# Performance work log

Measured on AMD Instinct MI355X. Metric: run time of the kernel, lower is better.

The kernel has to match this reference:

```python
import jax, jax.numpy as jnp
import numpy as np

B, T, H, D = 2, 2048, 8, 128
HID = H * D          # 1024
K_CONV = 4
EPS = 1e-5


def causal_dwconv(x, w, b):
    # x: [B,T,C], w: [C,K], b: [C]
    # torch Conv1d(groups=C, padding=K-1) followed by [..., :T] == left-padded causal depthwise conv
    K = w.shape[1]
    Tx = x.shape[1]
    xp = jnp.pad(x, ((0, 0), (K - 1, 0), (0, 0)))
    acc = jnp.zeros_like(x)
    for j in range(K):  # tiny fixed loop over kernel taps
        acc = acc + xp[:, j:j + Tx, :] * w[:, j]
    return acc + b


def setup_inputs() -> dict:
    key = jax.random.key(0)
    ks = jax.random.split(key, 16)
    s = 0.02
    inp = {
        'x':   jax.random.normal(ks[0], (B, T, HID), jnp.float32),
        'Wq':  s * jax.random.normal(ks[1], (HID, H * D), jnp.float32),
        'Wk':  s * jax.random.normal(ks[2], (HID, H * D), jnp.float32),
        'Wv':  s * jax.random.normal(ks[3], (HID, H * D), jnp.float32),
        'Wa':  s * jax.random.normal(ks[4], (HID, H * D), jnp.float32),
        'ba':  jnp.zeros((H * D,), jnp.float32),
        'Wb':  s * jax.random.normal(ks[5], (HID, H), jnp.float32),
        'bb':  jnp.zeros((H,), jnp.float32),
        'Wg':  s * jax.random.normal(ks[6], (HID, H * D), jnp.float32),
        'Wo':  s * jax.random.normal(ks[7], (H * D, HID), jnp.float32),
        'cqw': s * jax.random.normal(ks[8], (H * D, K_CONV), jnp.float32),
        'cqb': jnp.zeros((H * D,), jnp.float32),
        'ckw': s * jax.random.normal(ks[9], (H * D, K_CONV), jnp.float32),
        'ckb': jnp.zeros((H * D,), jnp.float32),
        'cvw': s * jax.random.normal(ks[10], (H * D, K_CONV), jnp.float32),
        'cvb': jnp.zeros((H * D,), jnp.float32),
        'ln_g': jnp.ones((D,), jnp.float32),
        'ln_b': jnp.zeros((D,), jnp.float32),
    }
    return inp


def reference(x, Wq, Wk, Wv, Wa, ba, Wb, bb, Wg, Wo,
              cqw, cqb, ckw, ckb, cvw, cvb, ln_g, ln_b):
    Bx, Tx, _ = x.shape
    q = x @ Wq
    k = x @ Wk
    v = x @ Wv
    q = jax.nn.silu(causal_dwconv(q, cqw, cqb))
    k = jax.nn.silu(causal_dwconv(k, ckw, ckb))
    v = jax.nn.silu(causal_dwconv(v, cvw, cvb))
    q = q.reshape(Bx, Tx, H, D)
    k = k.reshape(Bx, Tx, H, D) * (D ** -0.5)   # k scaled by head_dim_qk**-0.5
    v = v.reshape(Bx, Tx, H, D)
    a = jax.nn.sigmoid(x @ Wa + ba).reshape(Bx, Tx, H, D)
    beta = jax.nn.sigmoid(x @ Wb + bb)           # [B,T,H]

    # delta-rule recurrent scan; state S: [B,H,Dv,Dk]
    def step(S, inp):
        q_t, k_t, v_t, a_t, b_t = inp            # [B,H,D] / beta [B,H]
        delta = jnp.einsum('bhvk,bhk->bhv', S, k_t)
        err = delta - v_t
        S = a_t[..., None] * S - (b_t[..., None] * err)[..., None] * k_t[:, :, None, :]
        o_t = jnp.einsum('bhvk,bhk->bhv', S, q_t)
        return S, o_t

    tfirst = lambda z: jnp.moveaxis(z, 1, 0)     # [B,T,...] -> [T,B,...]
    S0 = jnp.zeros((Bx, H, D, D), x.dtype)
    _, o = jax.lax.scan(step, S0, (tfirst(q), tfirst(k), tfirst(v), tfirst(a), tfirst(beta)))
    o = jnp.moveaxis(o, 0, 1)                    # [B,T,H,D]

    # LayerNorm over head_dim_v
    mu = o.mean(-1, keepdims=True)
    var = ((o - mu) ** 2).mean(-1, keepdims=True)
    o = (o - mu) * jax.lax.rsqrt(var + EPS) * ln_g + ln_b

    g = jax.nn.sigmoid(x @ Wg).reshape(Bx, Tx, H, D)
    o = (o * g).reshape(Bx, Tx, H * D)
    return o @ Wo
```

## Files before the change

kernel.cpp:

```cpp
#include <hip/hip_runtime.h>
#include <hip/hip_bf16.h>
#include <cstdint>
#include <cstddef>

#define BATCH 2
#define TLEN  2048
#define NHEAD 8
#define HD    128
#define HIDN  1024
#define MTOT  4096
#define MAT_ELEMS 1048576
#define XELEMS 4194304
#define SCAN_C 32
#define NCH    64
#define SSC  1024.0f
#define ISSC 0.0009765625f

typedef _Float16 f16;
typedef _Float16 f16x2 __attribute__((ext_vector_type(2)));
typedef _Float16 f16x8 __attribute__((ext_vector_type(8)));
typedef float    f32x4 __attribute__((ext_vector_type(4)));

__device__ __forceinline__ float sigmoidf_(float v) { return 1.0f / (1.0f + __expf(-v)); }

// ... 191 lines not shown
{
    int ch = blockIdx.x;
    int bh = blockIdx.y;
    int b = bh >> 3, h = bh & 7;
    int lane = threadIdx.x;
    int L16 = lane & 15, quad = lane >> 4;
    size_t rowbase = (size_t)(b * TLEN) * HIDN + h * HD;
    int t0 = ch * SCAN_C;
    bool hasNext = (ch + 1 < NCH);

    union ZU { uint4 u; f16x8 v; };
    ZU zz; zz.u = (uint4){0, 0, 0, 0};

    f16x8 kc[2][4], qc[2][4], kn[2][4], qn[2][4];
#pragma unroll
    for (int nt = 0; nt < 2; ++nt)
#pragma unroll
        for (int kk = 0; kk < 4; ++kk) {
            size_t g = rowbase + (size_t)(t0 + nt * 16 + L16) * HIDN + kk * 32 + quad * 8;
            kc[nt][kk] = *(const f16x8*)(k16 + g);
            qc[nt][kk] = *(const f16x8*)(q16 + g);
            if (hasNext) {
                kn[nt][kk] = *(const f16x8*)(k16 + g + (size_t)SCAN_C * HIDN);
                qn[nt][kk] = *(const f16x8*)(q16 + g + (size_t)SCAN_C * HIDN);
            } else {
                kn[nt][kk] = zz.v; qn[nt][kk] = zz.v;
            }
        }

    f32x4 aG[2][2], aKQ[2][2], aGx[2][2], aQx[2][2];
#pragma unroll
    for (int i = 0; i < 2; ++i)
#pragma unroll
        for (int j = 0; j < 2; ++j) {
            aG[i][j] = (f32x4){0, 0, 0, 0}; aKQ[i][j] = (f32x4){0, 0, 0, 0};
            aGx[i][j] = (f32x4){0, 0, 0, 0}; aQx[i][j] = (f32x4){0, 0, 0, 0};
        }
#pragma unroll
    for (int kk = 0; kk < 4; ++kk)
#pragma unroll
        for (int mt = 0; mt < 2; ++mt)
#pragma unroll
            for (int nt = 0; nt < 2; ++nt) {
                aG[mt][nt]  = __builtin_amdgcn_mfma_f32_16x16x32_f16(kc[mt][kk], kc[nt][kk], aG[mt][nt], 0, 0, 0);
                aKQ[mt][nt] = __builtin_amdgcn_mfma_f32_16x16x32_f16(kc[mt][kk], qc[nt][kk], aKQ[mt][nt], 0, 0, 0);
                aGx[mt][nt] = __builtin_amdgcn_mfma_f32_16x16x32_f16(kc[mt][kk], kn[nt][kk], aGx[mt][nt], 0, 0, 0);
                aQx[mt][nt] = __builtin_amdgcn_mfma_f32_16x16x32_f16(kc[mt][kk], qn[nt][kk], aQx[mt][nt], 0, 0, 0);
            }

    size_t gb = ((size_t)bh * NCH + ch) * 1024;
#pragma unroll
    for (int nt = 0; nt < 2; ++nt) {
        int t = nt * 16 + L16;
#pragma unroll
        for (int mt = 0; mt < 2; ++mt) {
            union { f16 e[4]; uint2 u2; } pg, pq, px, py;
#pragma unroll
            for (int r = 0; r < 4; ++r) {
                pg.e[r] = (f16)aG[mt][nt][r];
                pq.e[r] = (f16)aKQ[mt][nt][r];
                px.e[r] = (f16)aGx[mt][nt][r];
                py.e[r] = (f16)aQx[mt][nt][r];
            }
            *(uint2*)(G_g  + gb + t * 32 + mt * 16 + quad * 4) = pg.u2;
            *(uint2*)(KQ_g + gb + t * 32 + mt * 16 + quad * 4) = pq.u2;
            *(uint2*)(Gx_g + gb + t * 32 + mt * 16 + quad * 4) = px.u2;
            *(uint2*)(Qx_g + gb + t * 32 + mt * 16 + quad * 4) = py.u2;
        }
    }
    size_t kb = ((size_t)bh * NCH + ch) * 4096;
#pragma unroll
    for (int nt = 0; nt < 2; ++nt) {
        int t = nt * 16 + L16;
#pragma unroll
        for (int kk = 0; kk < 4; ++kk)
#pragma unroll
            for (int j = 0; j < 8; ++j) {
                int k = kk * 32 + quad * 8 + j;
                KT_g[kb + (size_t)k * 32 + t] = kc[nt][kk][j];
            }
    }
}

__global__ __launch_bounds__(128, 1) void scan2_kernel(
    const f16* __restrict__ q16, const f16* __restrict__ k16, const f16* __restrict__ v16,
    const float* __restrict__ a_buf, const float* __restrict__ beta_buf,
    const f16* __restrict__ G_g, const f16* __restrict__ KQ_g,
    const f16* __restrict__ Gx_g, const f16* __restrict__ Qx_g, const f16* __restrict__ KT_g,
    float* __restrict__ o_buf)
{
    __shared__ __align__(16) float Sp[16 * 132];
    __shared__ __align__(16) f16   Sp16[16 * 136];
    __shared__ __align__(16) f16   KT_lds2[2][4096];
    __shared__ __align__(16) f16   G_lds[2][1024];
    __shared__ __align__(16) f16   Q_lds[2][1024];
    __shared__ __align__(16) f16   Gx_lds[2][1024];
    __shared__ __align__(16) f16   Qx_lds[2][1024];
    __shared__ __align__(16) float skv[2][16 * 34];
    __shared__ __align__(16) float sqv[2][16 * 34];
    __shared__ __align__(16) float avb[2][16 * 68];
    __shared__ __align__(16) float Bts[2][32];
    __shared__ __align__(16) f16   c16s[2][16 * 40];
    __shared__ __align__(16) float PCs[2][16];
    __shared__ __align__(16) float o_lds[2][16][34];

    const int tid = threadIdx.x;
    const int wid = tid >> 6;
    const int lane = tid & 63;
    const int L16 = lane & 15, quad = lane >> 4;
    const int vl = lane >> 2, li = lane & 3;
    const int t_av = lane >> 1, halfsel = lane & 1;

    const int bh = blockIdx.x;
    const int b = bh >> 3, h = bh & 7;
    const int v0 = blockIdx.y * 16;
    const size_t rowbase = (size_t)(b * TLEN) * HIDN + h * HD;
    const size_t gmatbase = (size_t)bh * NCH;

    {
        for (int i = tid; i < 16 * 132; i += 128) Sp[i] = 0.f;
        uint32_t* z;
        z = (uint32_t*)Sp16;    for (int i = tid; i < 16 * 136 / 2; i += 128) z[i] = 0u;
        z = (uint32_t*)KT_lds2; for (int i = tid; i < 2 * 4096 / 2; i += 128) z[i] = 0u;
        z = (uint32_t*)G_lds;   for (int i = tid; i < 1024;          i += 128) z[i] = 0u;
        z = (uint32_t*)Q_lds;   for (int i = tid; i < 1024;          i += 128) z[i] = 0u;
        z = (uint32_t*)Gx_lds;  for (int i = tid; i < 1024;          i += 128) z[i] = 0u;
        z = (uint32_t*)Qx_lds;  for (int i = tid; i < 1024;          i += 128) z[i] = 0u;
        z = (uint32_t*)skv;     for (int i = tid; i < 2 * 16 * 34;   i += 128) z[i] = 0u;
        z = (uint32_t*)sqv;     for (int i = tid; i < 2 * 16 * 34;   i += 128) z[i] = 0u;
        z = (uint32_t*)avb;     for (int i = tid; i < 2 * 16 * 68;   i += 128) z[i] = 0u;
        z = (uint32_t*)Bts;     for (int i = tid; i < 2 * 32;        i += 128) z[i] = 0u;
        z = (uint32_t*)c16s;    for (int i = tid; i < 2 * 16 * 40 / 2; i += 128) z[i] = 0u;
        z = (uint32_t*)PCs;     for (int i = tid; i < 2 * 16;        i += 128) z[i] = 0u;
    }
    __syncthreads();

    if (wid == 1) {
        f16x8 kfA[2][4], qfA[2][4], kfB[2][4], qfB[2][4];

        {
            size_t gb0 = gmatbase * 1024;
            *(uint4*)(&G_lds[0][lane * 16])     = *(const uint4*)(G_g  + gb0 + lane * 16);
            *(uint4*)(&G_lds[0][lane * 16 + 8]) = *(const uint4*)(G_g  + gb0 + lane * 16 + 8);
            *(uint4*)(&Q_lds[0][lane * 16])     = *(const uint4*)(KQ_g + gb0 + lane * 16);
            *(uint4*)(&Q_lds[0][lane * 16 + 8]) = *(const uint4*)(KQ_g + gb0 + lane * 16 + 8);
            size_t ga = rowbase + (size_t)t_av * HIDN + v0 + halfsel * 8;
            float4 ar0 = *(const float4*)(a_buf + ga);
            float4 ar1 = *(const float4*)(a_buf + ga + 4);
            uint4  vr  = *(const uint4*)(v16 + ga);
            float betr = beta_buf[((size_t)(b * TLEN) + t_av) * NHEAD + h];
            const f16* vh = (const f16*)&vr;
            const float* aa0 = (const float*)&ar0;
            const float* aa1 = (const float*)&ar1;
#pragma unroll
            for (int e = 0; e < 4; ++e) {
                float2 wv; wv.x = aa0[e]; wv.y = betr * (float)vh[e];
                *(float2*)(&avb[0][(halfsel * 8 + e) * 68 + 2 * t_av]) = wv;
                float2 wu; wu.x = aa1[e]; wu.y = betr * (float)vh[4 + e];
                *(float2*)(&avb[0][(halfsel * 8 + 4 + e) * 68 + 2 * t_av]) = wu;
            }
            if (halfsel == 0) Bts[0][t_av] = betr;
        }
        __syncthreads();

#define DO_UPDATE_MM(KF, QF)                                                        \
        if (ch >= 1 && ch <= NCH - 2) {                                             \
            f16x8 ca = *(const f16x8*)(&c16s[np][L16 * 40 + quad * 8]);             \
            float pc = PCs[np][L16];                                                \
            _Pragma("unroll")                                                       \
            for (int kt = 0; kt < 8; ++kt) {                                        \
                f16x8 bu = *(const f16x8*)(&KT_lds2[p][(kt * 16 + L16) * 32 + quad * 8]); \
                f32x4 d = __builtin_amdgcn_mfma_f32_16x16x32_f16(bu, ca, (f32x4){0, 0, 0, 0}, 0, 0, 0); \
                int idx = L16 * 132 + kt * 16 + quad * 4;                           \
                float4 s = *(const float4*)(&Sp[idx]);                              \
                s.x = fmaf(pc, s.x, d[0]);                                          \
                s.y = fmaf(pc, s.y, d[1]);                                          \
                s.z = fmaf(pc, s.z, d[2]);                                          \
                s.w = fmaf(pc, s.w, d[3]);                                          \
                *(float4*)(&Sp[idx]) = s;                                           \
                union { f16 e[4]; uint2 u2; } ph;                                   \
                ph.e[0] = (f16)s.x; ph.e[1] = (f16)s.y;                             \
                ph.e[2] = (f16)s.z; ph.e[3] = (f16)s.w;                             \
                *(uint2*)(&Sp16[L16 * 136 + kt * 16 + quad * 4]) = ph.u2;           \
            }                                                                       \
            f32x4 accK[2], accQ[2];                                                 \
            accK[0] = (f32x4){0, 0, 0, 0}; accK[1] = (f32x4){0, 0, 0, 0};           \
            accQ[0] = (f32x4){0, 0, 0, 0}; accQ[1] = (f32x4){0, 0, 0, 0};           \
            _Pragma("unroll")                                                       \
            for (int kk = 0; kk < 4; ++kk) {                                        \
                f16x8 sf = *(const f16x8*)(&Sp16[L16 * 136 + kk * 32 + quad * 8]);  \
                _Pragma("unroll")                                                   \
                for (int nt = 0; nt < 2; ++nt) {                                    \
                    accK[nt] = __builtin_amdgcn_mfma_f32_16x16x32_f16(sf, KF[nt][kk], accK[nt], 0, 0, 0); \
                    accQ[nt] = __builtin_amdgcn_mfma_f32_16x16x32_f16(sf, QF[nt][kk], accQ[nt], 0, 0, 0); \
                }                                                                   \
            }                                                                       \
            _Pragma("unroll")                                                       \
            for (int nt = 0; nt < 2; ++nt) {                                        \
                int t = nt * 16 + L16;                                              \
                _Pragma("unroll")                                                   \
                for (int r = 0; r < 4; ++r) {                                       \
                    skv[np][(quad * 4 + r) * 34 + t] = accK[nt][r];                 \
                    sqv[np][(quad * 4 + r) * 34 + t] = accQ[nt][r];                 \
                }                                                                   \
            }                                                                       \
        }

#define DO_PREFETCH(KF, QF)                                                         \
        if (ch <= NCH - 3) {                                                        \
            int tp = (ch + 2) * SCAN_C;                                             \
            _Pragma("unroll")                                                       \
            for (int nt = 0; nt < 2; ++nt)                                          \
                _Pragma("unroll")                                                   \
                for (int kk = 0; kk < 4; ++kk) {                                    \
                    size_t g = rowbase + (size_t)(tp + nt * 16 + L16) * HIDN + kk * 32 + quad * 8; \
                    KF[nt][kk] = *(const f16x8*)(k16 + g);                          \
                    QF[nt][kk] = *(const f16x8*)(q16 + g);                          \
                }                                                                   \
        }

        for (int ch = 0; ch < NCH; ++ch) {
            const int p = ch & 1;
            const int np = p ^ 1;
            const bool haveNext = (ch + 1 < NCH);

            float4 ar0, ar1; uint4 vr; float betr = 0.f;
            if (haveNext) {
                size_t gbn = (gmatbase + ch + 1) * 1024;
                size_t gbc = (gmatbase + ch) * 1024;
                const f16* gG = G_g  + gbn + lane * 8;
                const f16* gQ = KQ_g + gbn + lane * 8;
                const f16* gX = Gx_g + gbc + lane * 8;
                const f16* gY = Qx_g + gbc + lane * 8;
                gload_lds16(gG,       &G_lds[np][0]);
                gload_lds16(gG + 512, &G_lds[np][512]);
                gload_lds16(gQ,       &Q_lds[np][0]);
                gload_lds16(gQ + 512, &Q_lds[np][512]);
                gload_lds16(gX,       &Gx_lds[np][0]);
                gload_lds16(gX + 512, &Gx_lds[np][512]);
                gload_lds16(gY,       &Qx_lds[np][0]);
                gload_lds16(gY + 512, &Qx_lds[np][512]);
                const f16* gK = KT_g + (gmatbase + ch) * 4096 + lane * 8;
#pragma unroll
                for (int i = 0; i < 8; ++i)
                    gload_lds16(gK + i * 512, &KT_lds2[np][i * 512]);
                int tn = (ch + 1) * SCAN_C;
                size_t ga = rowbase + (size_t)(tn + t_av) * HIDN + v0 + halfsel * 8;
                ar0 = *(const float4*)(a_buf + ga);
                ar1 = *(const float4*)(a_buf + ga + 4);
                vr  = *(const uint4*)(v16 + ga);
                betr = beta_buf[((size_t)(b * TLEN) + tn + t_av) * NHEAD + h];
            }

            if ((ch & 1) == 0) { DO_PREFETCH(kfB, qfB) }
            else               { DO_PREFETCH(kfA, qfA) }

            if (ch >= 1) {
                const int fp = (ch - 1) & 1;
                const int tprev = (ch - 1) * SCAN_C;
                const int tt = lane >> 1;
                const int hh = (lane & 1) * 8;
                float v8[8];
#pragma unroll
                for (int j = 0; j < 8; ++j) v8[j] = o_lds[fp][hh + j][tt];
                float4 f0; f0.x = v8[0]; f0.y = v8[1]; f0.z = v8[2]; f0.w = v8[3];
                float4 f1; f1.x = v8[4]; f1.y = v8[5]; f1.z = v8[6]; f1.w = v8[7];
                size_t ob = rowbase + (size_t)(tprev + tt) * HIDN + v0 + hh;
                *(float4*)(o_buf + ob)     = f0;
                *(float4*)(o_buf + ob + 4) = f1;
            }

            if ((ch & 1) == 0) { DO_UPDATE_MM(kfA, qfA) }
            else               { DO_UPDATE_MM(kfB, qfB) }

            if (haveNext) {
                const f16* vh = (const f16*)&vr;
                const float* aa0 = (const float*)&ar0;
                const float* aa1 = (const float*)&ar1;
#pragma unroll
                for (int e = 0; e < 4; ++e) {
                    float2 wv; wv.x = aa0[e]; wv.y = betr * (float)vh[e];
                    *(float2*)(&avb[np][(halfsel * 8 + e) * 68 + 2 * t_av]) = wv;
                    float2 wu; wu.x = aa1[e]; wu.y = betr * (float)vh[4 + e];
                    *(float2*)(&avb[np][(halfsel * 8 + 4 + e) * 68 + 2 * t_av]) = wu;
                }
                if (halfsel == 0) Bts[np][t_av] = betr;
            }
            __syncthreads();
        }
#undef DO_UPDATE_MM
#undef DO_PREFETCH

        {
            const int fp = (NCH - 1) & 1;
            const int tprev = (NCH - 1) * SCAN_C;
            const int tt = lane >> 1;
            const int hh = (lane & 1) * 8;
            float v8[8];
#pragma unroll
            for (int j = 0; j < 8; ++j) v8[j] = o_lds[fp][hh + j][tt];
            float4 f0; f0.x = v8[0]; f0.y = v8[1]; f0.z = v8[2]; f0.w = v8[3];
            float4 f1; f1.x = v8[4]; f1.y = v8[5]; f1.z = v8[6]; f1.w = v8[7];
            size_t ob = rowbase + (size_t)(tprev + tt) * HIDN + v0 + hh;
            *(float4*)(o_buf + ob)     = f0;
            *(float4*)(o_buf + ob + 4) = f1;
        }
    } else {
        __builtin_amdgcn_s_setprio(1);
        __syncthreads();

        for (int ch = 0; ch < NCH; ++ch) {
            const int p = ch & 1;
            const int np = p ^ 1;

            {
                f16x8 caf = *(const f16x8*)(&c16s[np][L16 * 40 + quad * 8]);
                f32x4 fK[2], fQ[2];
#pragma unroll
                for (int nt = 0; nt < 2; ++nt) {
                    f16x8 bx = *(const f16x8*)(&Gx_lds[p][(nt * 16 + L16) * 32 + quad * 8]);
                    f16x8 by = *(const f16x8*)(&Qx_lds[p][(nt * 16 + L16) * 32 + quad * 8]);
                    fK[nt] = __builtin_amdgcn_mfma_f32_16x16x32_f16(caf, bx, (f32x4){0, 0, 0, 0}, 0, 0, 0);
                    fQ[nt] = __builtin_amdgcn_mfma_f32_16x16x32_f16(caf, by, (f32x4){0, 0, 0, 0}, 0, 0, 0);
                }
#pragma unroll
                for (int r = 0; r < 4; ++r) {
                    int vv = quad * 4 + r;
                    float Pv = PCs[np][vv];
#pragma unroll
                    for (int nt = 0; nt < 2; ++nt) {
                        int t = nt * 16 + L16;
                        skv[p][vv * 34 + t] = fmaf(Pv, skv[p][vv * 34 + t], fK[nt][r]);
                        sqv[p][vv * 34 + t] = fmaf(Pv, sqv[p][vv * 34 + t], fQ[nt][r]);
                    }
                }
            }

            {
                f16x2 c0, c1, c2, c3;
                c0.x = (f16)0.f; c0.y = (f16)0.f; c1 = c0; c2 = c0; c3 = c0;
                float P = 1.f;
                union RowU { uint4 u4; f16x2 h2[4]; };

                uint4  pg0[2], pg1[2], ph0[2], ph1[2];
                float2 pskp[2], psqp[2], pbtp[2];
                float4 pab4[2];
                float  pkq00[2], pg01[2];
                f16x2  pdq[2];

#define SOLVE_LD(SL, TT)                                                            \
                {                                                                   \
                    pg0[SL] = *(const uint4*)(&G_lds[p][(TT) * 32 + li * 8]);       \
                    pg1[SL] = *(const uint4*)(&G_lds[p][((TT) + 1) * 32 + li * 8]); \
                    ph0[SL] = *(const uint4*)(&Q_lds[p][(TT) * 32 + li * 8]);       \
                    ph1[SL] = *(const uint4*)(&Q_lds[p][((TT) + 1) * 32 + li * 8]); \
                    pskp[SL] = *(const float2*)(&skv[p][vl * 34 + (TT)]);           \
                    psqp[SL] = *(const float2*)(&sqv[p][vl * 34 + (TT)]);           \
                    pab4[SL] = *(const float4*)(&avb[p][vl * 68 + 2 * (TT)]);       \
                    pbtp[SL] = *(const float2*)(&Bts[p][(TT)]);                     \
                    pkq00[SL] = (float)Q_lds[p][(TT) * 32 + (TT)];                  \
                    pdq[SL]  = *(const f16x2*)(&Q_lds[p][((TT) + 1) * 32 + (TT)]);  \
                    pg01[SL] = (float)G_lds[p][((TT) + 1) * 32 + (TT)];             \
                }

                SOLVE_LD(0, 0)
                SOLVE_LD(1, 2)
#pragma unroll
                for (int t = 0; t < SCAN_C; t += 2) {
                    const int sl = (t >> 1) & 1;
                    RowU g0u, g1u, h0u, h1u;
                    g0u.u4 = pg0[sl]; g1u.u4 = pg1[sl];
                    h0u.u4 = ph0[sl]; h1u.u4 = ph1[sl];
                    float2 skp = pskp[sl], sqp = psqp[sl], btp = pbtp[sl];
                    float4 ab4 = pab4[sl];
                    float kq00 = pkq00[sl], g01 = pg01[sl];
                    f16x2 dq = pdq[sl];
                    if (t + 4 < SCAN_C) SOLVE_LD(sl, t + 4)

                    float pG  = fdot2_(c0, g0u.h2[0], fdot2_(c1, g0u.h2[1], 0.f))
                              + fdot2_(c2, g0u.h2[2], fdot2_(c3, g0u.h2[3], 0.f));
                    float pG1 = fdot2_(c0, g1u.h2[0], fdot2_(c1, g1u.h2[1], 0.f))
                              + fdot2_(c2, g1u.h2[2], fdot2_(c3, g1u.h2[3], 0.f));
                    float pO  = fdot2_(c0, h0u.h2[0], fdot2_(c1, h0u.h2[1], 0.f))
                              + fdot2_(c2, h0u.h2[2], fdot2_(c3, h0u.h2[3], 0.f));
                    float pO1 = fdot2_(c0, h1u.h2[0], fdot2_(c1, h1u.h2[1], 0.f))
                              + fdot2_(c2, h1u.h2[2], fdot2_(c3, h1u.h2[3], 0.f));
                    int tmp;
                    tmp = __builtin_amdgcn_update_dpp(0, __float_as_int(pG),  0xB1, 0xF, 0xF, true); pG  += __int_as_float(tmp);
                    tmp = __builtin_amdgcn_update_dpp(0, __float_as_int(pG1), 0xB1, 0xF, 0xF, true); pG1 += __int_as_float(tmp);
                    tmp = __builtin_amdgcn_update_dpp(0, __float_as_int(pO),  0xB1, 0xF, 0xF, true); pO  += __int_as_float(tmp);
                    tmp = __builtin_amdgcn_update_dpp(0, __float_as_int(pO1), 0xB1, 0xF, 0xF, true); pO1 += __int_as_float(tmp);
                    tmp = __builtin_amdgcn_update_dpp(0, __float_as_int(pG),  0x4E, 0xF, 0xF, true); pG  += __int_as_float(tmp);
                    tmp = __builtin_amdgcn_update_dpp(0, __float_as_int(pG1), 0x4E, 0xF, 0xF, true); pG1 += __int_as_float(tmp);
                    tmp = __builtin_amdgcn_update_dpp(0, __float_as_int(pO),  0x4E, 0xF, 0xF, true); pO  += __int_as_float(tmp);
                    tmp = __builtin_amdgcn_update_dpp(0, __float_as_int(pO1), 0x4E, 0xF, 0xF, true); pO1 += __int_as_float(tmp);

                    float a0 = ab4.x, bv0 = ab4.y, a1 = ab4.z, bv1 = ab4.w;
                    float bt0 = btp.x, bt1 = btp.y;
                    float sk0 = skp.x * ISSC, sk1 = skp.y * ISSC;
                    float sq0 = sqp.x * ISSC, sq1 = sqp.y * ISSC;
                    float kq01 = (float)dq.x, kq11 = (float)dq.y;

                    float x0 = fmaf(P, sk0, pG);
                    float u0 = fmaf(-bt0, x0, bv0);
                    float P0 = P * a0;
                    float o0 = fmaf(a0, pO, u0 * kq00);
                    o0 = fmaf(P0, sq0, o0);
                    float accGv = fmaf(a0, pG1, u0 * g01);
                    float x1 = fmaf(P0, sk1, accGv);
                    float u1 = fmaf(-bt1, x1, bv1);
                    float P1 = P0 * a1;
                    float accOv = fmaf(a0, pO1, u0 * kq01);
                    float o1 = fmaf(a1, accOv, u1 * kq11);
                    o1 = fmaf(P1, sq1, o1);

                    float aa = a0 * a1;
                    f16 aah = (f16)aa;
                    f16x2 aa2; aa2.x = aah; aa2.y = aah;
                    c0 *= aa2; c1 *= aa2; c2 *= aa2; c3 *= aa2;
                    if (li == (t >> 3)) {
                        f16x2 un; un.x = (f16)(u0 * a1); un.y = (f16)u1;
                        int sel = (t & 7) >> 1;
                        if (sel == 0) c0 = un; else if (sel == 1) c1 = un;
                        else if (sel == 2) c2 = un; else c3 = un;
                    }
                    P = P1;
                    if (li == 0) {
                        float2 o2; o2.x = o0; o2.y = o1;
                        *(float2*)(&o_lds[p][vl][t]) = o2;
                    }
                }
#undef SOLVE_LD
                f16 s16 = (f16)SSC;
                f16x2 ss2; ss2.x = s16; ss2.y = s16;
                union { f16x2 h2[4]; uint4 u4; } pc;
                pc.h2[0] = c0 * ss2; pc.h2[1] = c1 * ss2; pc.h2[2] = c2 * ss2; pc.h2[3] = c3 * ss2;
                *(uint4*)(&c16s[p][vl * 40 + li * 8]) = pc.u4;
                if (li == 0) PCs[p][vl] = P;
            }
            __syncthreads();
        }
    }
}

__global__ __launch_bounds__(256) void ln_gate_kernel(
    const float* __restrict__ o_buf, const f16* __restrict__ g16,
    const float* __restrict__ lng, const float* __restrict__ lnb,
    f16* __restrict__ og16)
{
    int row = blockIdx.x;
    int h = threadIdx.x >> 5, lane = threadIdx.x & 31;
    size_t base = (size_t)row * HIDN + h * HD + lane * 4;
    float4 x = *(const float4*)(o_buf + base);
    float s  = x.x + x.y + x.z + x.w;
    float sq = x.x * x.x + x.y * x.y + x.z * x.z + x.w * x.w;
#pragma unroll
    for (int m = 1; m <= 16; m <<= 1) {
        s  += __shfl_xor(s, m);
        sq += __shfl_xor(sq, m);
    }
    float mu  = s * (1.0f / 128.0f);
    float var = sq * (1.0f / 128.0f) - mu * mu;
    float inv = 1.0f / sqrtf(var + 1e-5f);
    int d = lane * 4;
    const float* xp = (const float*)&x;
    union { f16 h4[4]; uint2 u; } pk;
#pragma unroll
    for (int j = 0; j < 4; ++j) {
        float on = (xp[j] - mu) * inv * lng[d + j] + lnb[d + j];
        pk.h4[j] = (f16)(on * (float)g16[base + j]);
    }
    *(uint2*)(og16 + base) = pk.u;
}

extern "C" void kernel_launch(void* const* d_in, const int* in_sizes, int n_in,
                              void* d_out, int out_size, void* d_ws, size_t ws_size,
                              hipStream_t stream)
{
    (void)in_sizes; (void)n_in; (void)out_size; (void)ws_size;
    const float* x   = (const float*)d_in[0];
    const float* Wq  = (const float*)d_in[1];
    const float* Wk  = (const float*)d_in[2];
    const float* Wv  = (const float*)d_in[3];
    const float* Wa  = (const float*)d_in[4];
    const float* ba  = (const float*)d_in[5];
    const float* Wb  = (const float*)d_in[6];
    const float* bb  = (const float*)d_in[7];
    const float* Wg  = (const float*)d_in[8];
    const float* Wo  = (const float*)d_in[9];
    const float* cqw = (const float*)d_in[10];
    const float* cqb = (const float*)d_in[11];
    const float* ckw = (const float*)d_in[12];
    const float* ckb = (const float*)d_in[13];
    const float* cvw = (const float*)d_in[14];
    const float* cvb = (const float*)d_in[15];
    const float* lng = (const float*)d_in[16];
    const float* lnb = (const float*)d_in[17];
    float* out = (float*)d_out;

    char* ws = (char*)d_ws;
    f16*   x16      = (f16*)(ws + 0);
    f16*   WT       = (f16*)(ws + 8388608);
    f16*   qkvh     = (f16*)(ws + 20971520);
    f16*   qkv16    = (f16*)(ws + 46137344);
    float* a_buf    = (float*)(ws + 96468992);
    f16*   g16      = (f16*)(ws + 113246208);
    float* beta_buf = (float*)(ws + 121634816);
    float* o_buf    = (float*)(ws + 121765888);
    f16*   og16     = (f16*)(ws + 138543104);

    f16* G_g  = qkvh;
    f16* KQ_g = qkvh + 1048576;
    f16* Gx_g = qkvh + 2097152;
    f16* Qx_g = qkvh + 3145728;
    f16* KT_g = qkvh + 4194304;

    convert_x_kernel<<<dim3(4096), dim3(256), 0, stream>>>(x, x16);
    transpose_convert_kernel<<<dim3(32, 32, 6), dim3(256), 0, stream>>>(Wq, Wk, Wv, Wa, Wg, Wo, WT);
    gemm_f16<0><<<dim3(40, 32), dim3(256), 0, stream>>>(x16, WT, nullptr, qkvh, a_buf, g16, ba);
    beta_kernel<<<dim3(4096), dim3(256), 0, stream>>>(x, Wb, bb, beta_buf);
    conv_silu_kernel<<<dim3(4096, 3), dim3(256), 0, stream>>>(qkvh, cqw, cqb, ckw, ckb, cvw, cvb, qkv16);
    gram_kernel<<<dim3(NCH, 16), dim3(64), 0, stream>>>(
        qkv16, qkv16 + XELEMS, G_g, KQ_g, Gx_g, Qx_g, KT_g);
    scan2_kernel<<<dim3(16, 8), dim3(128), 0, stream>>>(
        qkv16, qkv16 + XELEMS, qkv16 + 2 * (size_t)XELEMS, a_buf, beta_buf,
        G_g, KQ_g, Gx_g, Qx_g, KT_g, o_buf);
    ln_gate_kernel<<<dim3(4096), dim3(256), 0, stream>>>(o_buf, g16, lng, lnb, og16);
    gemm_f16<1><<<dim3(8, 32), dim3(256), 0, stream>>>(og16, WT + 5 * (size_t)MAT_ELEMS, out,
                                                       nullptr, nullptr, nullptr, nullptr);
}
```

Measured before the change: 525.8 us.

## Warp-specialize scan kernel into solver, state-update, loader and IO waves

The scan kernel grows from two to four waves. Wave 1 previously did global loads, state updates and output stores itself; it now only does the MFMA state update. A new wave 2 prefetches G/KQ/Gx/Qx/KT tiles and stages the next chunk's k/q rows into a new padded LDS buffer instead of holding them in registers. A new wave 3 handles the a/v/beta loads and the o_buf writeback. The aim is to take global memory latency off the critical update path and to lower register pressure in the compute wave, at the cost of more LDS use, an extra LDS round trip for k/q, and four waves joining every per-chunk barrier.

After: 538.1 us. +2.3%, slower.

```diff
diff --git a/kernel.cpp b/kernel.cpp
--- a/kernel.cpp
+++ b/kernel.cpp
@@ -297,7 +297,7 @@
     }
 }
 
-__global__ __launch_bounds__(128, 1) void scan2_kernel(
+__global__ __launch_bounds__(256, 1) void scan2_kernel(
     const f16* __restrict__ q16, const f16* __restrict__ k16, const f16* __restrict__ v16,
     const float* __restrict__ a_buf, const float* __restrict__ beta_buf,
     const f16* __restrict__ G_g, const f16* __restrict__ KQ_g,
@@ -311,6 +311,7 @@
     __shared__ __align__(16) f16   Q_lds[2][1024];
     __shared__ __align__(16) f16   Gx_lds[2][1024];
     __shared__ __align__(16) f16   Qx_lds[2][1024];
+    __shared__ __align__(16) f16   kq_lds[2][2][32 * 136];
     __shared__ __align__(16) float skv[2][16 * 34];
     __shared__ __align__(16) float sqv[2][16 * 34];
     __shared__ __align__(16) float avb[2][16 * 68];
@@ -333,194 +334,25 @@
     const size_t gmatbase = (size_t)bh * NCH;
 
     {
-        for (int i = tid; i < 16 * 132; i += 128) Sp[i] = 0.f;
+        for (int i = tid; i < 16 * 132; i += 256) Sp[i] = 0.f;
         uint32_t* z;
-        z = (uint32_t*)Sp16;    for (int i = tid; i < 16 * 136 / 2; i += 128) z[i] = 0u;
-        z = (uint32_t*)KT_lds2; for (int i = tid; i < 2 * 4096 / 2; i += 128) z[i] = 0u;
-        z = (uint32_t*)G_lds;   for (int i = tid; i < 1024;          i += 128) z[i] = 0u;
-        z = (uint32_t*)Q_lds;   for (int i = tid; i < 1024;          i += 128) z[i] = 0u;
-        z = (uint32_t*)Gx_lds;  for (int i = tid; i < 1024;          i += 128) z[i] = 0u;
-        z = (uint32_t*)Qx_lds;  for (int i = tid; i < 1024;          i += 128) z[i] = 0u;
-        z = (uint32_t*)skv;     for (int i = tid; i < 2 * 16 * 34;   i += 128) z[i] = 0u;
-        z = (uint32_t*)sqv;     for (int i = tid; i < 2 * 16 * 34;   i += 128) z[i] = 0u;
-        z = (uint32_t*)avb;     for (int i = tid; i < 2 * 16 * 68;   i += 128) z[i] = 0u;
-        z = (uint32_t*)Bts;     for (int i = tid; i < 2 * 32;        i += 128) z[i] = 0u;
-        z = (uint32_t*)c16s;    for (int i = tid; i < 2 * 16 * 40 / 2; i += 128) z[i] = 0u;
-        z = (uint32_t*)PCs;     for (int i = tid; i < 2 * 16;        i += 128) z[i] = 0u;
+        z = (uint32_t*)Sp16;    for (int i = tid; i < 16 * 136 / 2; i += 256) z[i] = 0u;
+        z = (uint32_t*)KT_lds2; for (int i = tid; i < 2 * 4096 / 2; i += 256) z[i] = 0u;
+        z = (uint32_t*)G_lds;   for (int i = tid; i < 1024;          i += 256) z[i] = 0u;
+        z = (uint32_t*)Q_lds;   for (int i = tid; i < 1024;          i += 256) z[i] = 0u;
+        z = (uint32_t*)Gx_lds;  for (int i = tid; i < 1024;          i += 256) z[i] = 0u;
+        z = (uint32_t*)Qx_lds;  for (int i = tid; i < 1024;          i += 256) z[i] = 0u;
+        z = (uint32_t*)kq_lds;  for (int i = tid; i < 2 * 2 * 32 * 136 / 2; i += 256) z[i] = 0u;
+        z = (uint32_t*)skv;     for (int i = tid; i < 2 * 16 * 34;   i += 256) z[i] = 0u;
+        z = (uint32_t*)sqv;     for (int i = tid; i < 2 * 16 * 34;   i += 256) z[i] = 0u;
+        z = (uint32_t*)avb;     for (int i = tid; i < 2 * 16 * 68;   i += 256) z[i] = 0u;
+        z = (uint32_t*)Bts;     for (int i = tid; i < 2 * 32;        i += 256) z[i] = 0u;
+        z = (uint32_t*)c16s;    for (int i = tid; i < 2 * 16 * 40 / 2; i += 256) z[i] = 0u;
+        z = (uint32_t*)PCs;     for (int i = tid; i < 2 * 16;        i += 256) z[i] = 0u;
     }
     __syncthreads();
 
-    if (wid == 1) {
-        f16x8 kfA[2][4], qfA[2][4], kfB[2][4], qfB[2][4];
-
-        {
-            size_t gb0 = gmatbase * 1024;
-            *(uint4*)(&G_lds[0][lane * 16])     = *(const uint4*)(G_g  + gb0 + lane * 16);
-            *(uint4*)(&G_lds[0][lane * 16 + 8]) = *(const uint4*)(G_g  + gb0 + lane * 16 + 8);
-            *(uint4*)(&Q_lds[0][lane * 16])     = *(const uint4*)(KQ_g + gb0 + lane * 16);
-            *(uint4*)(&Q_lds[0][lane * 16 + 8]) = *(const uint4*)(KQ_g + gb0 + lane * 16 + 8);
-            size_t ga = rowbase + (size_t)t_av * HIDN + v0 + halfsel * 8;
-            float4 ar0 = *(const float4*)(a_buf + ga);
-            float4 ar1 = *(const float4*)(a_buf + ga + 4);
-            uint4  vr  = *(const uint4*)(v16 + ga);
-            float betr = beta_buf[((size_t)(b * TLEN) + t_av) * NHEAD + h];
-            const f16* vh = (const f16*)&vr;
-            const float* aa0 = (const float*)&ar0;
-            const float* aa1 = (const float*)&ar1;
-#pragma unroll
-            for (int e = 0; e < 4; ++e) {
-                float2 wv; wv.x = aa0[e]; wv.y = betr * (float)vh[e];
-                *(float2*)(&avb[0][(halfsel * 8 + e) * 68 + 2 * t_av]) = wv;
-                float2 wu; wu.x = aa1[e]; wu.y = betr * (float)vh[4 + e];
-                *(float2*)(&avb[0][(halfsel * 8 + 4 + e) * 68 + 2 * t_av]) = wu;
-            }
-            if (halfsel == 0) Bts[0][t_av] = betr;
-        }
-        __syncthreads();
-
-#define DO_UPDATE_MM(KF, QF)                                                        \
-        if (ch >= 1 && ch <= NCH - 2) {                                             \
-            f16x8 ca = *(const f16x8*)(&c16s[np][L16 * 40 + quad * 8]);             \
-            float pc = PCs[np][L16];                                                \
-            _Pragma("unroll")                                                       \
-            for (int kt = 0; kt < 8; ++kt) {                                        \
-                f16x8 bu = *(const f16x8*)(&KT_lds2[p][(kt * 16 + L16) * 32 + quad * 8]); \
-                f32x4 d = __builtin_amdgcn_mfma_f32_16x16x32_f16(bu, ca, (f32x4){0, 0, 0, 0}, 0, 0, 0); \
-                int idx = L16 * 132 + kt * 16 + quad * 4;                           \
-                float4 s = *(const float4*)(&Sp[idx]);                              \
-                s.x = fmaf(pc, s.x, d[0]);                                          \
-                s.y = fmaf(pc, s.y, d[1]);                                          \
-                s.z = fmaf(pc, s.z, d[2]);                                          \
-                s.w = fmaf(pc, s.w, d[3]);                                          \
-                *(float4*)(&Sp[idx]) = s;                                           \
-                union { f16 e[4]; uint2 u2; } ph;                                   \
-                ph.e[0] = (f16)s.x; ph.e[1] = (f16)s.y;                             \
-                ph.e[2] = (f16)s.z; ph.e[3] = (f16)s.w;                             \
-                *(uint2*)(&Sp16[L16 * 136 + kt * 16 + quad * 4]) = ph.u2;           \
-            }                                                                       \
-            f32x4 accK[2], accQ[2];                                                 \
-            accK[0] = (f32x4){0, 0, 0, 0}; accK[1] = (f32x4){0, 0, 0, 0};           \
-            accQ[0] = (f32x4){0, 0, 0, 0}; accQ[1] = (f32x4){0, 0, 0, 0};           \
-            _Pragma("unroll")                                                       \
-            for (int kk = 0; kk < 4; ++kk) {                                        \
-                f16x8 sf = *(const f16x8*)(&Sp16[L16 * 136 + kk * 32 + quad * 8]);  \
-                _Pragma("unroll")                                                   \
-                for (int nt = 0; nt < 2; ++nt) {                                    \
-                    accK[nt] = __builtin_amdgcn_mfma_f32_16x16x32_f16(sf, KF[nt][kk], accK[nt], 0, 0, 0); \
-                    accQ[nt] = __builtin_amdgcn_mfma_f32_16x16x32_f16(sf, QF[nt][kk], accQ[nt], 0, 0, 0); \
-                }                                                                   \
-            }                                                                       \
-            _Pragma("unroll")                                                       \
-            for (int nt = 0; nt < 2; ++nt) {                                        \
-                int t = nt * 16 + L16;                                              \
-                _Pragma("unroll")                                                   \
-                for (int r = 0; r < 4; ++r) {                                       \
-                    skv[np][(quad * 4 + r) * 34 + t] = accK[nt][r];                 \
-                    sqv[np][(quad * 4 + r) * 34 + t] = accQ[nt][r];                 \
-                }                                                                   \
-            }                                                                       \
-        }
-
-#define DO_PREFETCH(KF, QF)                                                         \
-        if (ch <= NCH - 3) {                                                        \
-            int tp = (ch + 2) * SCAN_C;                                             \
-            _Pragma("unroll")                                                       \
-            for (int nt = 0; nt < 2; ++nt)                                          \
-                _Pragma("unroll")                                                   \
-                for (int kk = 0; kk < 4; ++kk) {                                    \
-                    size_t g = rowbase + (size_t)(tp + nt * 16 + L16) * HIDN + kk * 32 + quad * 8; \
-                    KF[nt][kk] = *(const f16x8*)(k16 + g);                          \
-                    QF[nt][kk] = *(const f16x8*)(q16 + g);                          \
-                }                                                                   \
-        }
-
-        for (int ch = 0; ch < NCH; ++ch) {
-            const int p = ch & 1;
-            const int np = p ^ 1;
-            const bool haveNext = (ch + 1 < NCH);
-
-            float4 ar0, ar1; uint4 vr; float betr = 0.f;
-            if (haveNext) {
-                size_t gbn = (gmatbase + ch + 1) * 1024;
-                size_t gbc = (gmatbase + ch) * 1024;
-                const f16* gG = G_g  + gbn + lane * 8;
-                const f16* gQ = KQ_g + gbn + lane * 8;
-                const f16* gX = Gx_g + gbc + lane * 8;
-                const f16* gY = Qx_g + gbc + lane * 8;
-                gload_lds16(gG,       &G_lds[np][0]);
-                gload_lds16(gG + 512, &G_lds[np][512]);
-                gload_lds16(gQ,       &Q_lds[np][0]);
-                gload_lds16(gQ + 512, &Q_lds[np][512]);
-                gload_lds16(gX,       &Gx_lds[np][0]);
-                gload_lds16(gX + 512, &Gx_lds[np][512]);
-                gload_lds16(gY,       &Qx_lds[np][0]);
-                gload_lds16(gY + 512, &Qx_lds[np][512]);
-                const f16* gK = KT_g + (gmatbase + ch) * 4096 + lane * 8;
-#pragma unroll
-                for (int i = 0; i < 8; ++i)
-                    gload_lds16(gK + i * 512, &KT_lds2[np][i * 512]);
-                int tn = (ch + 1) * SCAN_C;
-                size_t ga = rowbase + (size_t)(tn + t_av) * HIDN + v0 + halfsel * 8;
-                ar0 = *(const float4*)(a_buf + ga);
-                ar1 = *(const float4*)(a_buf + ga + 4);
-                vr  = *(const uint4*)(v16 + ga);
-                betr = beta_buf[((size_t)(b * TLEN) + tn + t_av) * NHEAD + h];
-            }
-
-            if ((ch & 1) == 0) { DO_PREFETCH(kfB, qfB) }
-            else               { DO_PREFETCH(kfA, qfA) }
-
-            if (ch >= 1) {
-                const int fp = (ch - 1) & 1;
-                const int tprev = (ch - 1) * SCAN_C;
-                const int tt = lane >> 1;
-                const int hh = (lane & 1) * 8;
-                float v8[8];
-#pragma unroll
-                for (int j = 0; j < 8; ++j) v8[j] = o_lds[fp][hh + j][tt];
-                float4 f0; f0.x = v8[0]; f0.y = v8[1]; f0.z = v8[2]; f0.w = v8[3];
-                float4 f1; f1.x = v8[4]; f1.y = v8[5]; f1.z = v8[6]; f1.w = v8[7];
-                size_t ob = rowbase + (size_t)(tprev + tt) * HIDN + v0 + hh;
-                *(float4*)(o_buf + ob)     = f0;
-                *(float4*)(o_buf + ob + 4) = f1;
-            }
-
-            if ((ch & 1) == 0) { DO_UPDATE_MM(kfA, qfA) }
-            else               { DO_UPDATE_MM(kfB, qfB) }
-
-            if (haveNext) {
-                const f16* vh = (const f16*)&vr;
-                const float* aa0 = (const float*)&ar0;
-                const float* aa1 = (const float*)&ar1;
-#pragma unroll
-                for (int e = 0; e < 4; ++e) {
-                    float2 wv; wv.x = aa0[e]; wv.y = betr * (float)vh[e];
-                    *(float2*)(&avb[np][(halfsel * 8 + e) * 68 + 2 * t_av]) = wv;
-                    float2 wu; wu.x = aa1[e]; wu.y = betr * (float)vh[4 + e];
-                    *(float2*)(&avb[np][(halfsel * 8 + 4 + e) * 68 + 2 * t_av]) = wu;
-                }
-                if (halfsel == 0) Bts[np][t_av] = betr;
-            }
-            __syncthreads();
-        }
-#undef DO_UPDATE_MM
-#undef DO_PREFETCH
-
-        {
-            const int fp = (NCH - 1) & 1;
-            const int tprev = (NCH - 1) * SCAN_C;
-            const int tt = lane >> 1;
-            const int hh = (lane & 1) * 8;
-            float v8[8];
-#pragma unroll
-            for (int j = 0; j < 8; ++j) v8[j] = o_lds[fp][hh + j][tt];
-            float4 f0; f0.x = v8[0]; f0.y = v8[1]; f0.z = v8[2]; f0.w = v8[3];
-            float4 f1; f1.x = v8[4]; f1.y = v8[5]; f1.z = v8[6]; f1.w = v8[7];
-            size_t ob = rowbase + (size_t)(tprev + tt) * HIDN + v0 + hh;
-            *(float4*)(o_buf + ob)     = f0;
-            *(float4*)(o_buf + ob + 4) = f1;
-        }
-    } else {
+    if (wid == 0) {
         __builtin_amdgcn_s_setprio(1);
         __syncthreads();
 
@@ -654,6 +486,199 @@
                 if (li == 0) PCs[p][vl] = P;
             }
             __syncthreads();
+        }
+    } else if (wid == 1) {
+        __builtin_amdgcn_s_setprio(1);
+        __syncthreads();
+
+        for (int ch = 0; ch < NCH; ++ch) {
+            const int p = ch & 1;
+            const int np = p ^ 1;
+
+            if (ch >= 1 && ch <= NCH - 2) {
+                f16x8 ca = *(const f16x8*)(&c16s[np][L16 * 40 + quad * 8]);
+                float pc = PCs[np][L16];
+#pragma unroll
+                for (int kt = 0; kt < 8; ++kt) {
+                    f16x8 bu = *(const f16x8*)(&KT_lds2[p][(kt * 16 + L16) * 32 + quad * 8]);
+                    f32x4 d = __builtin_amdgcn_mfma_f32_16x16x32_f16(bu, ca, (f32x4){0, 0, 0, 0}, 0, 0, 0);
+                    int idx = L16 * 132 + kt * 16 + quad * 4;
+                    float4 s = *(const float4*)(&Sp[idx]);
+                    s.x = fmaf(pc, s.x, d[0]);
+                    s.y = fmaf(pc, s.y, d[1]);
+                    s.z = fmaf(pc, s.z, d[2]);
+                    s.w = fmaf(pc, s.w, d[3]);
+                    *(float4*)(&Sp[idx]) = s;
+                    union { f16 e[4]; uint2 u2; } ph;
+                    ph.e[0] = (f16)s.x; ph.e[1] = (f16)s.y;
+                    ph.e[2] = (f16)s.z; ph.e[3] = (f16)s.w;
+                    *(uint2*)(&Sp16[L16 * 136 + kt * 16 + quad * 4]) = ph.u2;
+                }
+                f32x4 accK[2], accQ[2];
+                accK[0] = (f32x4){0, 0, 0, 0}; accK[1] = (f32x4){0, 0, 0, 0};
+                accQ[0] = (f32x4){0, 0, 0, 0}; accQ[1] = (f32x4){0, 0, 0, 0};
+#pragma unroll
+                for (int kk = 0; kk < 4; ++kk) {
+                    f16x8 sf = *(const f16x8*)(&Sp16[L16 * 136 + kk * 32 + quad * 8]);
+#pragma unroll
+                    for (int nt = 0; nt < 2; ++nt) {
+                        f16x8 kfv = *(const f16x8*)(&kq_lds[p][0][(nt * 16 + L16) * 136 + kk * 32 + quad * 8]);
+                        f16x8 qfv = *(const f16x8*)(&kq_lds[p][1][(nt * 16 + L16) * 136 + kk * 32 + quad * 8]);
+                        accK[nt] = __builtin_amdgcn_mfma_f32_16x16x32_f16(sf, kfv, accK[nt], 0, 0, 0);
+                        accQ[nt] = __builtin_amdgcn_mfma_f32_16x16x32_f16(sf, qfv, accQ[nt], 0, 0, 0);
+                    }
+                }
+#pragma unroll
+                for (int nt = 0; nt < 2; ++nt) {
+                    int t = nt * 16 + L16;
+#pragma unroll
+                    for (int r = 0; r < 4; ++r) {
+                        skv[np][(quad * 4 + r) * 34 + t] = accK[nt][r];
+                        sqv[np][(quad * 4 + r) * 34 + t] = accQ[nt][r];
+                    }
+                }
+            }
+            __syncthreads();
+        }
+    } else if (wid == 2) {
+        {
+            size_t gb0 = gmatbase * 1024;
+            *(uint4*)(&G_lds[0][lane * 16])     = *(const uint4*)(G_g  + gb0 + lane * 16);
+            *(uint4*)(&G_lds[0][lane * 16 + 8]) = *(const uint4*)(G_g  + gb0 + lane * 16 + 8);
+            *(uint4*)(&Q_lds[0][lane * 16])     = *(const uint4*)(KQ_g + gb0 + lane * 16);
+            *(uint4*)(&Q_lds[0][lane * 16 + 8]) = *(const uint4*)(KQ_g + gb0 + lane * 16 + 8);
+        }
+        __syncthreads();
+
+        for (int ch = 0; ch < NCH; ++ch) {
+            const int np = (ch & 1) ^ 1;
+            const bool haveNext = (ch + 1 < NCH);
+            const bool doKQ = (ch <= NCH - 3);
+
+            f16x8 kreg[8], qreg[8];
+            if (doKQ) {
+                int tp2 = (ch + 2) * SCAN_C;
+#pragma unroll
+                for (int i = 0; i < 8; ++i) {
+                    int u = i * 64 + lane;
+                    int row = u >> 4, c8 = (u & 15) * 8;
+                    size_t g = rowbase + (size_t)(tp2 + row) * HIDN + c8;
+                    kreg[i] = *(const f16x8*)(k16 + g);
+                    qreg[i] = *(const f16x8*)(q16 + g);
+                }
+            }
+
+            if (haveNext) {
+                size_t gbn = (gmatbase + ch + 1) * 1024;
+                size_t gbc = (gmatbase + ch) * 1024;
+                const f16* gG = G_g  + gbn + lane * 8;
+                const f16* gQ = KQ_g + gbn + lane * 8;
+                const f16* gX = Gx_g + gbc + lane * 8;
+                const f16* gY = Qx_g + gbc + lane * 8;
+                gload_lds16(gG,       &G_lds[np][0]);
+                gload_lds16(gG + 512, &G_lds[np][512]);
+                gload_lds16(gQ,       &Q_lds[np][0]);
+                gload_lds16(gQ + 512, &Q_lds[np][512]);
+                gload_lds16(gX,       &Gx_lds[np][0]);
+                gload_lds16(gX + 512, &Gx_lds[np][512]);
+                gload_lds16(gY,       &Qx_lds[np][0]);
+                gload_lds16(gY + 512, &Qx_lds[np][512]);
+                const f16* gK = KT_g + (gmatbase + ch) * 4096 + lane * 8;
+#pragma unroll
+                for (int i = 0; i < 8; ++i)
+                    gload_lds16(gK + i * 512, &KT_lds2[np][i * 512]);
+            }
+
+            if (doKQ) {
+#pragma unroll
+                for (int i = 0; i < 8; ++i) {
+                    int u = i * 64 + lane;
+                    int row = u >> 4, c8 = (u & 15) * 8;
+                    *(f16x8*)(&kq_lds[np][0][row * 136 + c8]) = kreg[i];
+                    *(f16x8*)(&kq_lds[np][1][row * 136 + c8]) = qreg[i];
+                }
+            }
+            __syncthreads();
+        }
+    } else {
+        {
+            size_t ga = rowbase + (size_t)t_av * HIDN + v0 + halfsel * 8;
+            float4 ar0 = *(const float4*)(a_buf + ga);
+            float4 ar1 = *(const float4*)(a_buf + ga + 4);
+            uint4  vr  = *(const uint4*)(v16 + ga);
+            float betr = beta_buf[((size_t)(b * TLEN) + t_av) * NHEAD + h];
+            const f16* vh = (const f16*)&vr;
+            const float* aa0 = (const float*)&ar0;
+            const float* aa1 = (const float*)&ar1;
+#pragma unroll
+            for (int e = 0; e < 4; ++e) {
+                float2 wv; wv.x = aa0[e]; wv.y = betr * (float)vh[e];
+                *(float2*)(&avb[0][(halfsel * 8 + e) * 68 + 2 * t_av]) = wv;
+                float2 wu; wu.x = aa1[e]; wu.y = betr * (float)vh[4 + e];
+                *(float2*)(&avb[0][(halfsel * 8 + 4 + e) * 68 + 2 * t_av]) = wu;
+            }
+            if (halfsel == 0) Bts[0][t_av] = betr;
+        }
+        __syncthreads();
+
+        for (int ch = 0; ch < NCH; ++ch) {
+            const int np = (ch & 1) ^ 1;
+            const bool haveNext = (ch + 1 < NCH);
+
+            float4 ar0, ar1; uint4 vr; float betr = 0.f;
+            if (haveNext) {
+                int tn = (ch + 1) * SCAN_C;
+                size_t ga = rowbase + (size_t)(tn + t_av) * HIDN + v0 + halfsel * 8;
+                ar0 = *(const float4*)(a_buf + ga);
+                ar1 = *(const float4*)(a_buf + ga + 4);
+                vr  = *(const uint4*)(v16 + ga);
+                betr = beta_buf[((size_t)(b * TLEN) + tn + t_av) * NHEAD + h];
+            }
+
+            if (ch >= 1) {
+                const int fp = (ch - 1) & 1;
+                const int tprev = (ch - 1) * SCAN_C;
+                const int tt = lane >> 1;
+                const int hh = (lane & 1) * 8;
+                float v8[8];
+#pragma unroll
+                for (int j = 0; j < 8; ++j) v8[j] = o_lds[fp][hh + j][tt];
+                float4 f0; f0.x = v8[0]; f0.y = v8[1]; f0.z = v8[2]; f0.w = v8[3];
+                float4 f1; f1.x = v8[4]; f1.y = v8[5]; f1.z = v8[6]; f1.w = v8[7];
+                size_t ob = rowbase + (size_t)(tprev + tt) * HIDN + v0 + hh;
+                *(float4*)(o_buf + ob)     = f0;
+                *(float4*)(o_buf + ob + 4) = f1;
+            }
+
+            if (haveNext) {
+                const f16* vh = (const f16*)&vr;
+                const float* aa0 = (const float*)&ar0;
+                const float* aa1 = (const float*)&ar1;
+#pragma unroll
+                for (int e = 0; e < 4; ++e) {
+                    float2 wv; wv.x = aa0[e]; wv.y = betr * (float)vh[e];
+                    *(float2*)(&avb[np][(halfsel * 8 + e) * 68 + 2 * t_av]) = wv;
+                    float2 wu; wu.x = aa1[e]; wu.y = betr * (float)vh[4 + e];
+                    *(float2*)(&avb[np][(halfsel * 8 + 4 + e) * 68 + 2 * t_av]) = wu;
+                }
+                if (halfsel == 0) Bts[np][t_av] = betr;
+            }
+            __syncthreads();
+        }
+
+        {
+            const int fp = (NCH - 1) & 1;
+            const int tprev = (NCH - 1) * SCAN_C;
+            const int tt = lane >> 1;
+            const int hh = (lane & 1) * 8;
+            float v8[8];
+#pragma unroll
+            for (int j = 0; j < 8; ++j) v8[j] = o_lds[fp][hh + j][tt];
+            float4 f0; f0.x = v8[0]; f0.y = v8[1]; f0.z = v8[2]; f0.w = v8[3];
+            float4 f1; f1.x = v8[4]; f1.y = v8[5]; f1.z = v8[6]; f1.w = v8[7];
+            size_t ob = rowbase + (size_t)(tprev + tt) * HIDN + v0 + hh;
+            *(float4*)(o_buf + ob)     = f0;
+            *(float4*)(o_buf + ob + 4) = f1;
         }
     }
 }
@@ -737,7 +762,7 @@
     conv_silu_kernel<<<dim3(4096, 3), dim3(256), 0, stream>>>(qkvh, cqw, cqb, ckw, ckb, cvw, cvb, qkv16);
     gram_kernel<<<dim3(NCH, 16), dim3(64), 0, stream>>>(
         qkv16, qkv16 + XELEMS, G_g, KQ_g, Gx_g, Qx_g, KT_g);
-    scan2_kernel<<<dim3(16, 8), dim3(128), 0, stream>>>(
+    scan2_kernel<<<dim3(16, 8), dim3(256), 0, stream>>>(
         qkv16, qkv16 + XELEMS, qkv16 + 2 * (size_t)XELEMS, a_buf, beta_buf,
         G_g, KQ_g, Gx_g, Qx_g, KT_g, o_buf);
     ln_gate_kernel<<<dim3(4096), dim3(256), 0, stream>>>(o_buf, g16, lng, lnb, og16);
```

## Precompute next step's chunk dot products off the serial recurrence critical path

Applied to the files above, without the earlier changes.

The dot products of the running coefficient vector with the G and Q rows are now computed one step ahead, using the coefficients from before the newest update. The current step then corrects them with a cheap rank-2 scalar term (decay times the old dot plus the two newest u values times the diagonal-adjacent entries). This takes the fdot2 and DPP reduction chain off the serial dependency between u0/u1 and the next step, so it can overlap with the scalar recurrence. In exchange it adds extra LDS loads and register pressure. The correction path also uses the f16-rounded aa decay differently from the true c vector, which could cause small numeric drift.

Result: slower. 577.1 us (+9.8%).

```diff
diff --git a/kernel.cpp b/kernel.cpp
--- a/kernel.cpp
+++ b/kernel.cpp
@@ -555,6 +555,8 @@
                 f16x2 c0, c1, c2, c3;
                 c0.x = (f16)0.f; c0.y = (f16)0.f; c1 = c0; c2 = c0; c3 = c0;
                 float P = 1.f;
+                float dG0 = 0.f, dG1 = 0.f, dO0 = 0.f, dO1 = 0.f;
+                float uw0 = 0.f, uw1 = 0.f, aaP = 1.f;
                 union RowU { uint4 u4; f16x2 h2[4]; };
 
                 uint4  pg0[2], pg1[2], ph0[2], ph1[2];
@@ -562,6 +564,7 @@
                 float4 pab4[2];
                 float  pkq00[2], pg01[2];
                 f16x2  pdq[2];
+                f16x2  pcgx[2], pcgy[2], pcqx[2], pcqy[2];
 
 #define SOLVE_LD(SL, TT)                                                            \
                 {                                                                   \
@@ -576,6 +579,11 @@
                     pkq00[SL] = (float)Q_lds[p][(TT) * 32 + (TT)];                  \
                     pdq[SL]  = *(const f16x2*)(&Q_lds[p][((TT) + 1) * 32 + (TT)]);  \
                     pg01[SL] = (float)G_lds[p][((TT) + 1) * 32 + (TT)];             \
+                    const int cc_ = ((TT) >= 2) ? (TT) - 2 : 0;                     \
+                    pcgx[SL] = *(const f16x2*)(&G_lds[p][(TT) * 32 + cc_]);         \
+                    pcgy[SL] = *(const f16x2*)(&G_lds[p][((TT) + 1) * 32 + cc_]);   \
+                    pcqx[SL] = *(const f16x2*)(&Q_lds[p][(TT) * 32 + cc_]);         \
+                    pcqy[SL] = *(const f16x2*)(&Q_lds[p][((TT) + 1) * 32 + cc_]);   \
                 }
 
                 SOLVE_LD(0, 0)
@@ -583,32 +591,17 @@
 #pragma unroll
                 for (int t = 0; t < SCAN_C; t += 2) {
                     const int sl = (t >> 1) & 1;
-                    RowU g0u, g1u, h0u, h1u;
-                    g0u.u4 = pg0[sl]; g1u.u4 = pg1[sl];
-                    h0u.u4 = ph0[sl]; h1u.u4 = ph1[sl];
                     float2 skp = pskp[sl], sqp = psqp[sl], btp = pbtp[sl];
                     float4 ab4 = pab4[sl];
                     float kq00 = pkq00[sl], g01 = pg01[sl];
                     f16x2 dq = pdq[sl];
+                    f16x2 cgx = pcgx[sl], cgy = pcgy[sl], cqx = pcqx[sl], cqy = pcqy[sl];
                     if (t + 4 < SCAN_C) SOLVE_LD(sl, t + 4)
 
-                    float pG  = fdot2_(c0, g0u.h2[0], fdot2_(c1, g0u.h2[1], 0.f))
-                              + fdot2_(c2, g0u.h2[2], fdot2_(c3, g0u.h2[3], 0.f));
-                    float pG1 = fdot2_(c0, g1u.h2[0], fdot2_(c1, g1u.h2[1], 0.f))
-                              + fdot2_(c2, g1u.h2[2], fdot2_(c3, g1u.h2[3], 0.f));
-                    float pO  = fdot2_(c0, h0u.h2[0], fdot2_(c1, h0u.h2[1], 0.f))
-                              + fdot2_(c2, h0u.h2[2], fdot2_(c3, h0u.h2[3], 0.f));
-                    float pO1 = fdot2_(c0, h1u.h2[0], fdot2_(c1, h1u.h2[1], 0.f))
-                              + fdot2_(c2, h1u.h2[2], fdot2_(c3, h1u.h2[3], 0.f));
-                    int tmp;
-                    tmp = __builtin_amdgcn_update_dpp(0, __float_as_int(pG),  0xB1, 0xF, 0xF, true); pG  += __int_as_float(tmp);
-                    tmp = __builtin_amdgcn_update_dpp(0, __float_as_int(pG1), 0xB1, 0xF, 0xF, true); pG1 += __int_as_float(tmp);
-                    tmp = __builtin_amdgcn_update_dpp(0, __float_as_int(pO),  0xB1, 0xF, 0xF, true); pO  += __int_as_float(tmp);
-                    tmp = __builtin_amdgcn_update_dpp(0, __float_as_int(pO1), 0xB1, 0xF, 0xF, true); pO1 += __int_as_float(tmp);
-                    tmp = __builtin_amdgcn_update_dpp(0, __float_as_int(pG),  0x4E, 0xF, 0xF, true); pG  += __int_as_float(tmp);
-                    tmp = __builtin_amdgcn_update_dpp(0, __float_as_int(pG1), 0x4E, 0xF, 0xF, true); pG1 += __int_as_float(tmp);
-                    tmp = __builtin_amdgcn_update_dpp(0, __float_as_int(pO),  0x4E, 0xF, 0xF, true); pO  += __int_as_float(tmp);
-                    tmp = __builtin_amdgcn_update_dpp(0, __float_as_int(pO1), 0x4E, 0xF, 0xF, true); pO1 += __int_as_float(tmp);
+                    float pG   = fmaf(aaP, dG0, fmaf(uw0, (float)cgx.x, uw1 * (float)cgx.y));
+                    float pG1v = fmaf(aaP, dG1, fmaf(uw0, (float)cgy.x, uw1 * (float)cgy.y));
+                    float pO   = fmaf(aaP, dO0, fmaf(uw0, (float)cqx.x, uw1 * (float)cqx.y));
+                    float pO1v = fmaf(aaP, dO1, fmaf(uw0, (float)cqy.x, uw1 * (float)cqy.y));
 
                     float a0 = ab4.x, bv0 = ab4.y, a1 = ab4.z, bv1 = ab4.w;
                     float bt0 = btp.x, bt1 = btp.y;
@@ -621,13 +614,38 @@
                     float P0 = P * a0;
                     float o0 = fmaf(a0, pO, u0 * kq00);
                     o0 = fmaf(P0, sq0, o0);
-                    float accGv = fmaf(a0, pG1, u0 * g01);
+                    float accGv = fmaf(a0, pG1v, u0 * g01);
                     float x1 = fmaf(P0, sk1, accGv);
                     float u1 = fmaf(-bt1, x1, bv1);
                     float P1 = P0 * a1;
-                    float accOv = fmaf(a0, pO1, u0 * kq01);
+                    float accOv = fmaf(a0, pO1v, u0 * kq01);
                     float o1 = fmaf(a1, accOv, u1 * kq11);
                     o1 = fmaf(P1, sq1, o1);
+
+                    if (t + 2 < SCAN_C) {
+                        const int so = sl ^ 1;
+                        RowU g0u, g1u, h0u, h1u;
+                        g0u.u4 = pg0[so]; g1u.u4 = pg1[so];
+                        h0u.u4 = ph0[so]; h1u.u4 = ph1[so];
+                        float nG0 = fdot2_(c0, g0u.h2[0], fdot2_(c1, g0u.h2[1], 0.f))
+                                  + fdot2_(c2, g0u.h2[2], fdot2_(c3, g0u.h2[3], 0.f));
+                        float nG1 = fdot2_(c0, g1u.h2[0], fdot2_(c1, g1u.h2[1], 0.f))
+                                  + fdot2_(c2, g1u.h2[2], fdot2_(c3, g1u.h2[3], 0.f));
+                        float nO0 = fdot2_(c0, h0u.h2[0], fdot2_(c1, h0u.h2[1], 0.f))
+                                  + fdot2_(c2, h0u.h2[2], fdot2_(c3, h0u.h2[3], 0.f));
+                        float nO1 = fdot2_(c0, h1u.h2[0], fdot2_(c1, h1u.h2[1], 0.f))
+                                  + fdot2_(c2, h1u.h2[2], fdot2_(c3, h1u.h2[3], 0.f));
+                        int tmp;
+                        tmp = __builtin_amdgcn_update_dpp(0, __float_as_int(nG0), 0xB1, 0xF, 0xF, true); nG0 += __int_as_float(tmp);
+                        tmp = __builtin_amdgcn_update_dpp(0, __float_as_int(nG1), 0xB1, 0xF, 0xF, true); nG1 += __int_as_float(tmp);
+                        tmp = __builtin_amdgcn_update_dpp(0, __float_as_int(nO0), 0xB1, 0xF, 0xF, true); nO0 += __int_as_float(tmp);
+                        tmp = __builtin_amdgcn_update_dpp(0, __float_as_int(nO1), 0xB1, 0xF, 0xF, true); nO1 += __int_as_float(tmp);
+                        tmp = __builtin_amdgcn_update_dpp(0, __float_as_int(nG0), 0x4E, 0xF, 0xF, true); nG0 += __int_as_float(tmp);
+                        tmp = __builtin_amdgcn_update_dpp(0, __float_as_int(nG1), 0x4E, 0xF, 0xF, true); nG1 += __int_as_float(tmp);
+                        tmp = __builtin_amdgcn_update_dpp(0, __float_as_int(nO0), 0x4E, 0xF, 0xF, true); nO0 += __int_as_float(tmp);
+                        tmp = __builtin_amdgcn_update_dpp(0, __float_as_int(nO1), 0x4E, 0xF, 0xF, true); nO1 += __int_as_float(tmp);
+                        dG0 = nG0; dG1 = nG1; dO0 = nO0; dO1 = nO1;
+                    }
 
                     float aa = a0 * a1;
                     f16 aah = (f16)aa;
@@ -639,6 +657,7 @@
                         if (sel == 0) c0 = un; else if (sel == 1) c1 = un;
                         else if (sel == 2) c2 = un; else c3 = un;
                     }
+                    uw0 = u0 * a1; uw1 = u1; aaP = aa;
                     P = P1;
                     if (li == 0) {
                         float2 o2; o2.x = o0; o2.y = o1;
```
